# Kernel tuning notes

Hardware: AMD Instinct MI355X
Metric: run time of the kernel (lower is better)

Reference implementation:

```python
import jax, jax.numpy as jnp
import numpy as np

N_NODES = 10000
N_EDGES = 320000


def _segment_softmax(scores, seg, num_segments):
    # scores: [E, H], segment-wise stable softmax keyed by seg (edge_index[0])
    m = jax.ops.segment_max(scores, seg, num_segments=num_segments)
    e = jnp.exp(scores - m[seg])
    z = jax.ops.segment_sum(e, seg, num_segments=num_segments)
    return e / z[seg]


def _gat_layer(x, W, a, row, col, n_nodes, heads, out_dim):
    # x: [N, F_in], W: [F_in, heads*out_dim], a: [heads, 2*out_dim]
    h = (x @ W).reshape(n_nodes, heads, out_dim)          # [N, H, F]
    a_l, a_r = a[:, :out_dim], a[:, out_dim:]             # [H, F] each
    # attention score per edge/head without materializing [E, H, 2F]
    s = (h[row] * a_l).sum(-1) + (h[col] * a_r).sum(-1)   # [E, H]
    alpha = _segment_softmax(s, row, n_nodes)             # [E, H]
    msg = alpha[..., None] * h[row]                       # [E, H, F]
    return jax.ops.segment_sum(msg, col, num_segments=n_nodes)  # [N, H, F]


def setup_inputs() -> dict:
    key = jax.random.key(0)
    ks = jax.random.split(key, 6)
    F, H, C = 128, 4, 22
    x = jax.random.normal(ks[0], (N_NODES, F), dtype=jnp.float32)
    edge_index = jax.random.randint(ks[1], (2, N_EDGES), 0, N_NODES, dtype=jnp.int64)
    W1 = jax.random.normal(ks[2], (F, F * H), dtype=jnp.float32) * 0.05
    a1 = jax.random.normal(ks[3], (H, 2 * F), dtype=jnp.float32) * 0.05
    W2 = jax.random.normal(ks[4], (F, C), dtype=jnp.float32) * 0.05
    a2 = jax.random.normal(ks[5], (1, 2 * C), dtype=jnp.float32) * 0.05
    return {"x": x, "edge_index": edge_index, "W1": W1, "a1": a1, "W2": W2, "a2": a2}


def reference(x, edge_index, W1, a1, W2, a2):
    row, col = edge_index[0], edge_index[1]
    h1 = _gat_layer(x, W1, a1, row, col, N_NODES, heads=4, out_dim=128)  # [N, 4, 128]
    h1 = jax.nn.elu(h1).mean(axis=1)                                      # combine heads -> [N, 128]
    h2 = _gat_layer(h1, W2, a2, row, col, N_NODES, heads=1, out_dim=22)   # [N, 1, 22]
    return h2[:, 0, :]                                                    # [N, 22]
```

## Files before the change

kernel.cpp:

```cpp
#include <hip/hip_runtime.h>

#define NN 10000
#define NE 320000
#define EPP 5000
#define NPART 64

typedef short short8 __attribute__((ext_vector_type(8)));
typedef float f32x4 __attribute__((ext_vector_type(4)));

__device__ __forceinline__ unsigned short f2bf(float f) {
    unsigned u = __float_as_uint(f);
    return (unsigned short)((u + 0x7FFFu + ((u >> 16) & 1u)) >> 16);
}
__device__ __forceinline__ float bflo(unsigned v) { return __uint_as_float(v << 16); }
__device__ __forceinline__ float bfhi(unsigned v) { return __uint_as_float(v & 0xffff0000u); }
__device__ __forceinline__ float bf1(unsigned short v) { return __uint_as_float(((unsigned)v) << 16); }

__device__ __forceinline__ int eread(const void* p, int is64, int i) {
    if (is64) return (int)((const long long*)p)[i];
    return ((const int*)p)[i];
}

__device__ __forceinline__ int detect64(const void* ei) {
    const unsigned* idx = (const unsigned*)ei;
    int all0 = 1;
    for (int j = 1; j < 257; j += 2)
        if (idx[j] != 0u) { all0 = 0; break; }
    return all0;
}

__global__ __launch_bounds__(256) void k_pre(const float* __restrict__ x,
                                             unsigned short* __restrict__ xb,
                                             const void* __restrict__ ei,
                                             unsigned short* __restrict__ degp_c,
                                             unsigned short* __restrict__ degp_r,
                                             unsigned* __restrict__ packed_c,
                                             unsigned* __restrict__ packed_r,
                                             const float* __restrict__ W1, const float* __restrict__ a1,
                                             unsigned short* __restrict__ W1t,
                                             float* __restrict__ wrf) {
    __shared__ int sh[NN];
    const int b = blockIdx.x, t = threadIdx.x;
    if (b < 2500) {
        const int g = b * 256 + t;
        const float2 v = *(const float2*)&x[(size_t)g * 2];
        ushort2 o; o.x = f2bf(v.x); o.y = f2bf(v.y);
        *(ushort2*)&xb[(size_t)g * 2] = o;
    } else if (b < 2500 + 2 * NPART) {
        const int is64 = detect64(ei);
        const int isC = (b < 2500 + NPART);
        const int p = isC ? (b - 2500) : (b - 2500 - NPART);
        const int ebase = p * EPP;
        for (int q = t; q < NN; q += 256) sh[q] = 0;
        __syncthreads();
        if (isC) {
            for (int q = t; q < EPP; q += 256) {
                const int e = ebase + q;
                const int c = eread(ei, is64, NE + e);
                const unsigned rk = (unsigned)atomicAdd(&sh[c], 1);
                packed_c[e] = ((unsigned)c << 13) | rk;
            }
            __syncthreads();
            for (int q = t; q < NN; q += 256) degp_c[p * NN + q] = (unsigned short)sh[q];
        } else {
            for (int q = t; q < EPP; q += 256) {
                const int e = ebase + q;
                const int r = eread(ei, is64, e);
                const unsigned rk = (unsigned)atomicAdd(&sh[r], 1);
                packed_r[e] = ((unsigned)r << 13) | rk;
            }
            __syncthreads();
            for (int q = t; q < NN; q += 256) degp_r[p * NN + q] = (unsigned short)sh[q];
        }
    } else if (b < 2500 + 2 * NPART + 256) {
        const int g = (b - 2500 - 2 * NPART) * 256 + t;
        const int h = g >> 14, j = (g >> 7) & 127, k = g & 127;
        W1t[g] = f2bf(W1[(size_t)k * 512 + h * 128 + j]);
    } else {
        const int g = (b - 2500 - 2 * NPART - 256) * 256 + t;
        const int h = g >> 7, k = g & 127;
        const float* wrow = W1 + (size_t)k * 512 + h * 128;
        const float* av = a1 + h * 256 + 128;
        float s = 0.f;
        for (int d = 0; d < 128; d++) s += wrow[d] * av[d];
        wrf[h * 128 + k] = s;
    }
}

__global__ __launch_bounds__(256) void k_psum(const unsigned short* __restrict__ degp_c,
                                              const unsigned short* __restrict__ degp_r,
                                              unsigned short* __restrict__ pfx_c,
                                              unsigned short* __restrict__ pfx_r,
                                              int* __restrict__ deg_c, int* __restrict__ deg_r) {
    const int g = blockIdx.x * 256 + threadIdx.x;
    if (g >= 2 * NN) return;
    const int arr = g / NN, node = g % NN;
    const unsigned short* degp = arr ? degp_r : degp_c;
    unsigned short* pfx = arr ? pfx_r : pfx_c;
    int* tot = arr ? deg_r : deg_c;
    int sum = 0;
#pragma unroll
    for (int p = 0; p < NPART; p++) {
        pfx[p * NN + node] = (unsigned short)sum;
        sum += (int)degp[p * NN + node];
    }
    tot[node] = sum;
}

__device__ void scan_one_1k(const int* __restrict__ deg, int* __restrict__ start, int* ssum) {
    const int t = threadIdx.x;
    int loc[10];
    const int base = t * 10;
    int sum = 0;
#pragma unroll
    for (int j = 0; j < 10; j++) {
        int i = base + j;
        int v = (i < NN) ? deg[i] : 0;
        loc[j] = sum;
        sum += v;
    }
    const int lane = t & 63, w = t >> 6;
    int xi = sum;
#pragma unroll
    for (int off = 1; off < 64; off <<= 1) {
        int y = __shfl_up(xi, off);
        if (lane >= off) xi += y;
    }
    __syncthreads();
    if (lane == 63) ssum[w] = xi;
    __syncthreads();
    int woff = 0;
#pragma unroll
    for (int k = 0; k < 16; k++)
        if (k < w) woff += ssum[k];
    const int excl = woff + xi - sum;
#pragma unroll
    for (int j = 0; j < 10; j++) {
        int i = base + j;
        if (i < NN) start[i] = excl + loc[j];
    }
}

__global__ __launch_bounds__(1024) void k_scan2(const int* __restrict__ deg_c, const int* __restrict__ deg_r,
                                                int* __restrict__ start_c, int* __restrict__ start_r) {
    __shared__ int ssum[16];
    scan_one_1k(deg_c, start_c, ssum);
    __syncthreads();
    scan_one_1k(deg_r, start_r, ssum);
}

__global__ __launch_bounds__(256) void k_build(const unsigned* __restrict__ packed_c,
                                               const unsigned* __restrict__ packed_r,
                                               const unsigned short* __restrict__ pfx_c,
                                               const unsigned short* __restrict__ pfx_r,
                                               const int* __restrict__ start_c, const int* __restrict__ start_r,
                                               int* __restrict__ csrA, int* __restrict__ csrB,
                                               const float* __restrict__ x, const float* __restrict__ wrf,
                                               float* __restrict__ ehr1) {
    __shared__ float ls[512];
    const int b = blockIdx.x, t = threadIdx.x;
    if (b < 1250) {
        const int e = b * 256 + t;
        const int part = e / EPP;
        const unsigned pc = packed_c[e], pr = packed_r[e];
        const int c = (int)(pc >> 13), rkc = (int)(pc & 8191u);
        const int r = (int)(pr >> 13), rkr = (int)(pr & 8191u);
        csrA[start_c[c] + (int)pfx_c[part * NN + c] + rkc] = r;
        csrB[start_r[r] + (int)pfx_r[part * NN + r] + rkr] = c;
    } else {
        const int lane = t & 63, w = t >> 6;
        ls[t] = wrf[t];
        ls[t + 256] = wrf[t + 256];
        __syncthreads();
        const int i = (b - 1250) * 4 + w;
        const float x0 = x[(size_t)i * 128 + lane];
        const float x1 = x[(size_t)i * 128 + 64 + lane];
        float v[4];
#pragma unroll
        for (int h = 0; h < 4; h++)
            v[h] = x0 * ls[h * 128 + lane] + x1 * ls[h * 128 + 64 + lane];
#pragma unroll
        for (int off = 1; off < 64; off <<= 1) {
#pragma unroll
            for (int j = 0; j < 4; j++) v[j] += __shfl_xor(v[j], off);
        }
        if (lane == 0)
            *(float4*)&ehr1[i * 4] = make_float4(__expf(v[0]), __expf(v[1]), __expf(v[2]), __expf(v[3]));
    }
}

__global__ __launch_bounds__(256) void k_z1(const int* __restrict__ start_r, const int* __restrict__ deg_r,
                                            const int* __restrict__ csrB,
                                            const float* __restrict__ ehr1, float* __restrict__ rz1) {
    const int t = threadIdx.x, lane = t & 63, w = t >> 6;
    const int half = lane >> 5, l32 = lane & 31;
    const int i = blockIdx.x * 8 + w * 2 + half;
    const int s0 = start_r[i], d = deg_r[i];
    float zx = 0.f, zy = 0.f, zz = 0.f, zw = 0.f;
    for (int p = s0 + l32; p < s0 + d; p += 32) {
        const int c = csrB[p];
        const float4 v = *(const float4*)&ehr1[c * 4];
        zx += v.x; zy += v.y; zz += v.z; zw += v.w;
    }
#pragma unroll
    for (int off = 1; off < 32; off <<= 1) {
        zx += __shfl_xor(zx, off); zy += __shfl_xor(zy, off);
        zz += __shfl_xor(zz, off); zw += __shfl_xor(zw, off);
    }
    if (l32 == 0)
        *(float4*)&rz1[i * 4] = make_float4(1.f / zx, 1.f / zy, 1.f / zz, 1.f / zw);
}

__global__ __launch_bounds__(1024) void k_aggF(const unsigned short* __restrict__ xb,
                                               const float* __restrict__ ehr1, const float* __restrict__ rz1,
                                               const int* __restrict__ start_c, const int* __restrict__ deg_c,
                                               const int* __restrict__ csrA,
                                               const unsigned short* __restrict__ W1t,
                                               const float* __restrict__ W2, const float* __restrict__ a2,
                                               float* __restrict__ h2, float* __restrict__ ehr2) {
    __shared__ unsigned short lx[16 * 512];
    __shared__ float h1f[16 * 128];
    __shared__ float w2s[2816];
    __shared__ float a2s[22];
    const int t = threadIdx.x, lane = t & 63, w = t >> 6;
    const int n0 = blockIdx.x * 16;

    for (int q = t; q < 2816; q += 1024) w2s[q] = W2[q];
    if (t < 22) a2s[t] = a2[22 + t];

    {
        const int i = n0 + w;
        const float4 er4 = *(const float4*)&ehr1[i * 4];
        const int s0 = start_c[i], dg = deg_c[i];
        float acc[8];
#pragma unroll
        for (int j = 0; j < 8; j++) acc[j] = 0.f;
        int p = s0;
        const int e8 = s0 + (dg & ~7);
        for (; p < e8; p += 8) {
            int rr[8]; unsigned vv[8]; float4 zz[8];
#pragma unroll
            for (int q = 0; q < 8; q++) rr[q] = csrA[p + q];
#pragma unroll
            for (int q = 0; q < 8; q++) vv[q] = *(const unsigned*)&xb[(size_t)rr[q] * 128 + lane * 2];
#pragma unroll
            for (int q = 0; q < 8; q++) zz[q] = *(const float4*)&rz1[rr[q] * 4];
#pragma unroll
            for (int q = 0; q < 8; q++) {
                const float xa = bflo(vv[q]), xbv = bfhi(vv[q]);
                acc[0] += zz[q].x * xa; acc[1] += zz[q].x * xbv;
                acc[2] += zz[q].y * xa; acc[3] += zz[q].y * xbv;
                acc[4] += zz[q].z * xa; acc[5] += zz[q].z * xbv;
                acc[6] += zz[q].w * xa; acc[7] += zz[q].w * xbv;
            }
        }
        for (; p < s0 + dg; ++p) {
            const int r = csrA[p];
            const unsigned v = *(const unsigned*)&xb[(size_t)r * 128 + lane * 2];
            const float4 z = *(const float4*)&rz1[r * 4];
            const float xa = bflo(v), xbv = bfhi(v);
            acc[0] += z.x * xa; acc[1] += z.x * xbv;
            acc[2] += z.y * xa; acc[3] += z.y * xbv;
            acc[4] += z.z * xa; acc[5] += z.z * xbv;
            acc[6] += z.w * xa; acc[7] += z.w * xbv;
        }
        const float ef[4] = {er4.x, er4.y, er4.z, er4.w};
        const int fin = (lane & 3) * 2;
#pragma unroll
        for (int h = 0; h < 4; h++) {
            const int f = h * 16 + (lane >> 2);
            const int sc = ((f ^ (w & 7)) << 3) + fin;
            ushort2 st;
            st.x = f2bf(acc[h * 2] * ef[h]);
            st.y = f2bf(acc[h * 2 + 1] * ef[h]);
            *(ushort2*)&lx[w * 512 + sc] = st;
        }
    }
    __syncthreads();

    if (w < 8) {
        const int j = w;
        const int r16 = lane & 15, grp = lane >> 4;
        f32x4 hm = (f32x4)0.f;
#pragma unroll
        for (int h = 0; h < 4; h++) {
            f32x4 acc = (f32x4)0.f;
#pragma unroll
            for (int kk = 0; kk < 128; kk += 32) {
                const int f = h * 16 + (kk >> 3) + grp;
                const int sc = (f ^ (r16 & 7)) << 3;
                short8 a = *(const short8*)&lx[r16 * 512 + sc];
                short8 bfr = *(const short8*)&W1t[(size_t)h * 16384 + (j * 16 + r16) * 128 + kk + grp * 8];
                acc = __builtin_amdgcn_mfma_f32_16x16x32_bf16(a, bfr, acc, 0, 0, 0);
            }
#pragma unroll
            for (int r = 0; r < 4; r++) {
                const float v = acc[r];
                hm[r] += (v > 0.f) ? v : (__expf(v) - 1.f);
            }
        }
#pragma unroll
        for (int r = 0; r < 4; r++)
            h1f[(grp * 4 + r) * 128 + j * 16 + r16] = 0.25f * hm[r];
    }
    __syncthreads();

    {
        const int i = n0 + w;
        const int seg = lane >> 5, c = lane & 31;
        float part = 0.f;
        if (c < 22) {
            const float* hrow = &h1f[w * 128 + seg * 64];
            const float* wp = &w2s[seg * 64 * 22 + c];
            for (int k = 0; k < 64; k++)
                part += hrow[k] * wp[k * 22];
        }
        part += __shfl_xor(part, 32);
        if (lane < 22) h2[(size_t)i * 22 + lane] = part;
        float pr = (lane < 22) ? part * a2s[lane] : 0.f;
#pragma unroll
        for (int off = 1; off < 64; off <<= 1)
            pr += __shfl_xor(pr, off);
        if (lane == 0) ehr2[i] = __expf(pr);
    }
}

__global__ __launch_bounds__(256) void k_z2s(const int* __restrict__ start_r, const int* __restrict__ deg_r,
                                             const int* __restrict__ csrB,
                                             const float* __restrict__ ehr2, const float* __restrict__ h2,
                                             unsigned short* __restrict__ h2s) {
    const int t = threadIdx.x, lane = t & 63, w = t >> 6;
    const int half = lane >> 5, l32 = lane & 31;
    const int i = blockIdx.x * 8 + w * 2 + half;
    const int s0 = start_r[i], d = deg_r[i];
    float z = 0.f;
    for (int p = s0 + l32; p < s0 + d; p += 32)
        z += ehr2[csrB[p]];
#pragma unroll
    for (int off = 1; off < 32; off <<= 1)
        z += __shfl_xor(z, off);
    const float rz = 1.f / z;
    if (l32 < 22)
        h2s[(size_t)i * 32 + l32] = f2bf(h2[(size_t)i * 22 + l32] * rz);
}

__global__ __launch_bounds__(256) void k_agg2(const unsigned short* __restrict__ h2s,
                                              const float* __restrict__ ehr2,
                                              const int* __restrict__ start_c, const int* __restrict__ deg_c,
                                              const int* __restrict__ csrA,
                                              float* __restrict__ out) {
    const int t = threadIdx.x, lane = t & 63, w = t >> 6;
    const int half = lane >> 5, c32 = lane & 31;
    const int i = blockIdx.x * 8 + w * 2 + half;
    const int s0 = start_c[i], dg = deg_c[i];
    const float e2 = ehr2[i];
    const int c = (c32 < 22) ? c32 : 0;
    float acc = 0.f;
    int p = s0;
    const int e8 = s0 + (dg & ~7);
    for (; p < e8; p += 8) {
        int rr[8];
#pragma unroll
        for (int q = 0; q < 8; q++) rr[q] = csrA[p + q];
        float vv[8];
#pragma unroll
        for (int q = 0; q < 8; q++) vv[q] = bf1(h2s[(size_t)rr[q] * 32 + c]);
#pragma unroll
        for (int q = 0; q < 8; q++) acc += vv[q];
    }
    for (; p < s0 + dg; ++p) {
        const int r = csrA[p];
        acc += bf1(h2s[(size_t)r * 32 + c]);
    }
    if (c32 < 22) out[(size_t)i * 22 + c32] = acc * e2;
}

extern "C" void kernel_launch(void* const* d_in, const int* in_sizes, int n_in,
                              void* d_out, int out_size, void* d_ws, size_t ws_size,
                              hipStream_t stream) {
    const float* x  = (const float*)d_in[0];
    const void*  ei = d_in[1];
    const float* W1 = (const float*)d_in[2];
    const float* a1 = (const float*)d_in[3];
    const float* W2 = (const float*)d_in[4];
    const float* a2 = (const float*)d_in[5];
    float* out = (float*)d_out;

    float* ws = (float*)d_ws;
    float* h2   = ws;
    float* ehr1 = ws + 220000;
    float* rz1  = ws + 260000;
    float* ehr2 = ws + 300000;
    unsigned short* h2s = (unsigned short*)(ws + 310000);
    int* deg_c   = (int*)(ws + 470000);
    int* deg_r   = (int*)(ws + 480000);
    int* start_c = (int*)(ws + 490000);
    int* start_r = (int*)(ws + 500000);
    int* csrA    = (int*)(ws + 510000);
    int* csrB    = (int*)(ws + 830000);
    float* wrf   = ws + 1150000;
    unsigned short* W1t = (unsigned short*)(ws + 1151000);
    unsigned short* xb  = (unsigned short*)(ws + 1184000);
    unsigned* packed_c = (unsigned*)(ws + 1824000);
    unsigned* packed_r = (unsigned*)(ws + 2144000);
    unsigned short* degp_c = (unsigned short*)(ws + 2464000);
    unsigned short* degp_r = (unsigned short*)(ws + 2784000);
    unsigned short* pfx_c  = (unsigned short*)(ws + 3104000);
    unsigned short* pfx_r  = (unsigned short*)(ws + 3424000);

    k_pre<<<2500 + 2 * NPART + 258, 256, 0, stream>>>(x, xb, ei, degp_c, degp_r,
                                                      packed_c, packed_r, W1, a1, W1t, wrf);
    k_psum<<<79, 256, 0, stream>>>(degp_c, degp_r, pfx_c, pfx_r, deg_c, deg_r);
    k_scan2<<<1, 1024, 0, stream>>>(deg_c, deg_r, start_c, start_r);
    k_build<<<3750, 256, 0, stream>>>(packed_c, packed_r, pfx_c, pfx_r,
                                      start_c, start_r, csrA, csrB, x, wrf, ehr1);
    k_z1<<<1250, 256, 0, stream>>>(start_r, deg_r, csrB, ehr1, rz1);
    k_aggF<<<625, 1024, 0, stream>>>(xb, ehr1, rz1, start_c, deg_c, csrA, W1t,
                                     W2, a2, h2, ehr2);
    k_z2s<<<1250, 256, 0, stream>>>(start_r, deg_r, csrB, ehr2, h2, h2s);
    k_agg2<<<1250, 256, 0, stream>>>(h2s, ehr2, start_c, deg_c, csrA, out);
}
```

Measured before the change: 104.1 us.

## Shrink k_aggF to 256 threads with 16-lane-per-node gathers and uint4 loads

```diff
diff --git a/kernel.cpp b/kernel.cpp
--- a/kernel.cpp
+++ b/kernel.cpp
@@ -211,117 +211,136 @@
         *(float4*)&rz1[i * 4] = make_float4(1.f / zx, 1.f / zy, 1.f / zz, 1.f / zw);
 }
 
-__global__ __launch_bounds__(1024) void k_aggF(const unsigned short* __restrict__ xb,
-                                               const float* __restrict__ ehr1, const float* __restrict__ rz1,
-                                               const int* __restrict__ start_c, const int* __restrict__ deg_c,
-                                               const int* __restrict__ csrA,
-                                               const unsigned short* __restrict__ W1t,
-                                               const float* __restrict__ W2, const float* __restrict__ a2,
-                                               float* __restrict__ h2, float* __restrict__ ehr2) {
+__global__ __launch_bounds__(256) void k_aggF(const unsigned short* __restrict__ xb,
+                                              const float* __restrict__ ehr1, const float* __restrict__ rz1,
+                                              const int* __restrict__ start_c, const int* __restrict__ deg_c,
+                                              const int* __restrict__ csrA,
+                                              const unsigned short* __restrict__ W1t,
+                                              const float* __restrict__ W2, const float* __restrict__ a2,
+                                              float* __restrict__ h2, float* __restrict__ ehr2) {
     __shared__ unsigned short lx[16 * 512];
     __shared__ float h1f[16 * 128];
-    __shared__ float w2s[2816];
-    __shared__ float a2s[22];
     const int t = threadIdx.x, lane = t & 63, w = t >> 6;
     const int n0 = blockIdx.x * 16;
 
-    for (int q = t; q < 2816; q += 1024) w2s[q] = W2[q];
-    if (t < 22) a2s[t] = a2[22 + t];
-
     {
-        const int i = n0 + w;
+        const int li = lane & 15, g = lane >> 4;
+        const int row = w * 4 + g;
+        const int i = n0 + row;
         const float4 er4 = *(const float4*)&ehr1[i * 4];
         const int s0 = start_c[i], dg = deg_c[i];
-        float acc[8];
-#pragma unroll
-        for (int j = 0; j < 8; j++) acc[j] = 0.f;
-        int p = s0;
-        const int e8 = s0 + (dg & ~7);
-        for (; p < e8; p += 8) {
-            int rr[8]; unsigned vv[8]; float4 zz[8];
-#pragma unroll
-            for (int q = 0; q < 8; q++) rr[q] = csrA[p + q];
-#pragma unroll
-            for (int q = 0; q < 8; q++) vv[q] = *(const unsigned*)&xb[(size_t)rr[q] * 128 + lane * 2];
-#pragma unroll
-            for (int q = 0; q < 8; q++) zz[q] = *(const float4*)&rz1[rr[q] * 4];
-#pragma unroll
-            for (int q = 0; q < 8; q++) {
-                const float xa = bflo(vv[q]), xbv = bfhi(vv[q]);
-                acc[0] += zz[q].x * xa; acc[1] += zz[q].x * xbv;
-                acc[2] += zz[q].y * xa; acc[3] += zz[q].y * xbv;
-                acc[4] += zz[q].z * xa; acc[5] += zz[q].z * xbv;
-                acc[6] += zz[q].w * xa; acc[7] += zz[q].w * xbv;
-            }
-        }
-        for (; p < s0 + dg; ++p) {
-            const int r = csrA[p];
-            const unsigned v = *(const unsigned*)&xb[(size_t)r * 128 + lane * 2];
-            const float4 z = *(const float4*)&rz1[r * 4];
-            const float xa = bflo(v), xbv = bfhi(v);
-            acc[0] += z.x * xa; acc[1] += z.x * xbv;
-            acc[2] += z.y * xa; acc[3] += z.y * xbv;
-            acc[4] += z.z * xa; acc[5] += z.z * xbv;
-            acc[6] += z.w * xa; acc[7] += z.w * xbv;
+        int m = dg;
+        m = max(m, __shfl_xor(m, 16));
+        m = max(m, __shfl_xor(m, 32));
+        float acc[4][8];
+#pragma unroll
+        for (int h = 0; h < 4; h++)
+#pragma unroll
+            for (int d = 0; d < 8; d++) acc[h][d] = 0.f;
+        const int niter = (m + 3) >> 2;
+        for (int it = 0; it < niter; ++it) {
+            const int base = it * 4;
+            int rr[4]; uint4 vv[4]; float4 zz[4];
+#pragma unroll
+            for (int q = 0; q < 4; q++) {
+                int p = s0 + base + q;
+                if (p >= NE) p = NE - 1;
+                rr[q] = csrA[p];
+            }
+#pragma unroll
+            for (int q = 0; q < 4; q++)
+                vv[q] = *(const uint4*)&xb[(size_t)rr[q] * 128 + li * 8];
+#pragma unroll
+            for (int q = 0; q < 4; q++) {
+                const float4 z = *(const float4*)&rz1[rr[q] * 4];
+                const bool val = (base + q) < dg;
+                zz[q] = val ? z : make_float4(0.f, 0.f, 0.f, 0.f);
+            }
+#pragma unroll
+            for (int q = 0; q < 4; q++) {
+                float f[8];
+                f[0] = bflo(vv[q].x); f[1] = bfhi(vv[q].x);
+                f[2] = bflo(vv[q].y); f[3] = bfhi(vv[q].y);
+                f[4] = bflo(vv[q].z); f[5] = bfhi(vv[q].z);
+                f[6] = bflo(vv[q].w); f[7] = bfhi(vv[q].w);
+                const float wz0 = zz[q].x, wz1 = zz[q].y, wz2 = zz[q].z, wz3 = zz[q].w;
+#pragma unroll
+                for (int d = 0; d < 8; d++) {
+                    acc[0][d] += wz0 * f[d];
+                    acc[1][d] += wz1 * f[d];
+                    acc[2][d] += wz2 * f[d];
+                    acc[3][d] += wz3 * f[d];
+                }
+            }
         }
         const float ef[4] = {er4.x, er4.y, er4.z, er4.w};
-        const int fin = (lane & 3) * 2;
 #pragma unroll
         for (int h = 0; h < 4; h++) {
-            const int f = h * 16 + (lane >> 2);
-            const int sc = ((f ^ (w & 7)) << 3) + fin;
-            ushort2 st;
-            st.x = f2bf(acc[h * 2] * ef[h]);
-            st.y = f2bf(acc[h * 2 + 1] * ef[h]);
-            *(ushort2*)&lx[w * 512 + sc] = st;
+            unsigned o[4];
+#pragma unroll
+            for (int d2 = 0; d2 < 4; d2++) {
+                const unsigned lo = f2bf(acc[h][d2 * 2] * ef[h]);
+                const unsigned hi = f2bf(acc[h][d2 * 2 + 1] * ef[h]);
+                o[d2] = lo | (hi << 16);
+            }
+            const int f = h * 16 + li;
+            const int sc = (f ^ (row & 7)) << 3;
+            *(uint4*)&lx[row * 512 + sc] = make_uint4(o[0], o[1], o[2], o[3]);
         }
     }
     __syncthreads();
 
-    if (w < 8) {
-        const int j = w;
+    {
         const int r16 = lane & 15, grp = lane >> 4;
-        f32x4 hm = (f32x4)0.f;
-#pragma unroll
-        for (int h = 0; h < 4; h++) {
-            f32x4 acc = (f32x4)0.f;
-#pragma unroll
-            for (int kk = 0; kk < 128; kk += 32) {
-                const int f = h * 16 + (kk >> 3) + grp;
-                const int sc = (f ^ (r16 & 7)) << 3;
-                short8 a = *(const short8*)&lx[r16 * 512 + sc];
-                short8 bfr = *(const short8*)&W1t[(size_t)h * 16384 + (j * 16 + r16) * 128 + kk + grp * 8];
-                acc = __builtin_amdgcn_mfma_f32_16x16x32_bf16(a, bfr, acc, 0, 0, 0);
-            }
-#pragma unroll
-            for (int r = 0; r < 4; r++) {
-                const float v = acc[r];
-                hm[r] += (v > 0.f) ? v : (__expf(v) - 1.f);
-            }
-        }
-#pragma unroll
-        for (int r = 0; r < 4; r++)
-            h1f[(grp * 4 + r) * 128 + j * 16 + r16] = 0.25f * hm[r];
+#pragma unroll
+        for (int jj = 0; jj < 2; jj++) {
+            const int j = w * 2 + jj;
+            f32x4 hm = (f32x4)0.f;
+#pragma unroll
+            for (int h = 0; h < 4; h++) {
+                f32x4 acc = (f32x4)0.f;
+#pragma unroll
+                for (int kk = 0; kk < 128; kk += 32) {
+                    const int f = h * 16 + (kk >> 3) + grp;
+                    const int sc = (f ^ (r16 & 7)) << 3;
+                    short8 a = *(const short8*)&lx[r16 * 512 + sc];
+                    short8 bfr = *(const short8*)&W1t[(size_t)h * 16384 + (j * 16 + r16) * 128 + kk + grp * 8];
+                    acc = __builtin_amdgcn_mfma_f32_16x16x32_bf16(a, bfr, acc, 0, 0, 0);
+                }
+#pragma unroll
+                for (int r = 0; r < 4; r++) {
+                    const float v = acc[r];
+                    hm[r] += (v > 0.f) ? v : (__expf(v) - 1.f);
+                }
+            }
+#pragma unroll
+            for (int r = 0; r < 4; r++)
+                h1f[(grp * 4 + r) * 128 + j * 16 + r16] = 0.25f * hm[r];
+        }
     }
     __syncthreads();
 
     {
-        const int i = n0 + w;
         const int seg = lane >> 5, c = lane & 31;
-        float part = 0.f;
-        if (c < 22) {
-            const float* hrow = &h1f[w * 128 + seg * 64];
-            const float* wp = &w2s[seg * 64 * 22 + c];
-            for (int k = 0; k < 64; k++)
-                part += hrow[k] * wp[k * 22];
-        }
-        part += __shfl_xor(part, 32);
-        if (lane < 22) h2[(size_t)i * 22 + lane] = part;
-        float pr = (lane < 22) ? part * a2s[lane] : 0.f;
-#pragma unroll
-        for (int off = 1; off < 64; off <<= 1)
-            pr += __shfl_xor(pr, off);
-        if (lane == 0) ehr2[i] = __expf(pr);
+#pragma unroll
+        for (int q = 0; q < 4; q++) {
+            const int nl = w * 4 + q;
+            const int i = n0 + nl;
+            float part = 0.f;
+            if (c < 22) {
+                const float* hrow = &h1f[nl * 128 + seg * 64];
+                const float* wp = &W2[seg * 64 * 22 + c];
+                for (int k = 0; k < 64; k++)
+                    part += hrow[k] * wp[k * 22];
+            }
+            part += __shfl_xor(part, 32);
+            if (lane < 22) h2[(size_t)i * 22 + lane] = part;
+            float pr = (lane < 22) ? part * a2[22 + lane] : 0.f;
+#pragma unroll
+            for (int off = 1; off < 64; off <<= 1)
+                pr += __shfl_xor(pr, off);
+            if (lane == 0) ehr2[i] = __expf(pr);
+        }
     }
 }
 
@@ -415,8 +434,8 @@
     k_build<<<3750, 256, 0, stream>>>(packed_c, packed_r, pfx_c, pfx_r,
                                       start_c, start_r, csrA, csrB, x, wrf, ehr1);
     k_z1<<<1250, 256, 0, stream>>>(start_r, deg_r, csrB, ehr1, rz1);
-    k_aggF<<<625, 1024, 0, stream>>>(xb, ehr1, rz1, start_c, deg_c, csrA, W1t,
-                                     W2, a2, h2, ehr2);
+    k_aggF<<<625, 256, 0, stream>>>(xb, ehr1, rz1, start_c, deg_c, csrA, W1t,
+                                    W2, a2, h2, ehr2);
     k_z2s<<<1250, 256, 0, stream>>>(start_r, deg_r, csrB, ehr2, h2, h2s);
     k_agg2<<<1250, 256, 0, stream>>>(h2s, ehr2, start_c, deg_c, csrA, out);
 }
```

After: 99.33 us (median of 2 runs). 1.05x faster.
